# Optimization experiments

Measured on AMD Instinct MI355X. Metric: run time of the kernel, lower is better.

Reference implementation:

```python
import jax, jax.numpy as jnp
import numpy as np

FRAME_SIZE = 160

def _gru(x, h0, wih, whh, bih, bhh):
    # x: [B,T,D], h0: [B,U]; torch GRU gate order: r, z, n
    xp = jnp.einsum('btd,gd->btg', x, wih) + bih  # [B,T,3U]
    def step(h, xt):
        hp = h @ whh.T + bhh
        xr, xz, xn = jnp.split(xt, 3, axis=-1)
        hr, hz, hn = jnp.split(hp, 3, axis=-1)
        r = jax.nn.sigmoid(xr + hr)
        z = jax.nn.sigmoid(xz + hz)
        n = jnp.tanh(xn + r * hn)
        h_new = (1.0 - z) * n + z * h
        return h_new, h_new
    hT, ys = jax.lax.scan(step, h0, jnp.swapaxes(xp, 0, 1))
    return jnp.swapaxes(ys, 0, 1), hT

def _conv1d(x, w, b):
    # x: [B,C,T], w: [O,I,K], valid padding
    y = jax.lax.conv_general_dilated(x, w, (1,), 'VALID', dimension_numbers=('NCH', 'OIH', 'NCH'))
    return y + b[None, :, None]

def setup_inputs() -> dict:
    key = jax.random.key(0)
    ks = jax.random.split(key, 24)
    B, T, FD = 16, 36, 20
    PE, CD, K = 64, 128, 3
    SE, UA, UB, OUT = 128, 384, 64, 256
    NS = 3
    S = (T - 2 * (K - 1)) * FRAME_SIZE  # 32 * 160 = 5120
    s = 0.05
    inp = {
        'features': jax.random.normal(ks[0], (B, T, FD), jnp.float32),
        'periods': jax.random.randint(ks[1], (B, T, 1), 0, 256),
        'signals': jax.random.randint(ks[2], (B, S, NS), 0, 256),
        'gru_a_state': jnp.zeros((B, UA), jnp.float32),
        'gru_b_state': jnp.zeros((B, UB), jnp.float32),
        'period_emb': jax.random.normal(ks[3], (256, PE), jnp.float32) * s,
        'signal_emb': jax.random.normal(ks[4], (256, SE), jnp.float32) * s,
        'conv1_w': jax.random.normal(ks[5], (CD, FD + PE, K), jnp.float32) * s,
        'conv1_b': jnp.zeros((CD,), jnp.float32),
        'conv2_w': jax.random.normal(ks[6], (CD, CD, K), jnp.float32) * s,
        'conv2_b': jnp.zeros((CD,), jnp.float32),
        'fd1_w': jax.random.normal(ks[7], (CD, CD), jnp.float32) * s,
        'fd1_b': jnp.zeros((CD,), jnp.float32),
        'fd2_w': jax.random.normal(ks[8], (CD, CD), jnp.float32) * s,
        'fd2_b': jnp.zeros((CD,), jnp.float32),
        'grua_wih': jax.random.normal(ks[9], (3 * UA, NS * SE + CD), jnp.float32) * s,
        'grua_whh': jax.random.normal(ks[10], (3 * UA, UA), jnp.float32) * s,
        'grua_bih': jnp.zeros((3 * UA,), jnp.float32),
        'grua_bhh': jnp.zeros((3 * UA,), jnp.float32),
        'grub_wih': jax.random.normal(ks[11], (3 * UB, UA + CD), jnp.float32) * s,
        'grub_whh': jax.random.normal(ks[12], (3 * UB, UB), jnp.float32) * s,
        'grub_bih': jnp.zeros((3 * UB,), jnp.float32),
        'grub_bhh': jnp.zeros((3 * UB,), jnp.float32),
        'fc1_w': jax.random.normal(ks[13], (OUT, UB), jnp.float32) * s,
        'fc1_b': jnp.zeros((OUT,), jnp.float32),
        'fc2_w': jax.random.normal(ks[14], (OUT, UB), jnp.float32) * s,
        'fc2_b': jnp.zeros((OUT,), jnp.float32),
        'alpha': jnp.ones((OUT,), jnp.float32),
        'beta': jnp.ones((OUT,), jnp.float32),
    }
    return inp

def reference(features, periods, signals, gru_a_state, gru_b_state, period_emb,
              signal_emb, conv1_w, conv1_b, conv2_w, conv2_b, fd1_w, fd1_b,
              fd2_w, fd2_b, grua_wih, grua_whh, grua_bih, grua_bhh, grub_wih,
              grub_whh, grub_bih, grub_bhh, fc1_w, fc1_b, fc2_w, fc2_b, alpha, beta):
    B = features.shape[0]
    # ---- frame rate network ----
    ep = period_emb[periods].reshape(B, periods.shape[1], -1)  # [B,T,PE]
    f = jnp.concatenate([features, ep], axis=-1)               # [B,T,FD+PE]
    c = jnp.transpose(f, (0, 2, 1))                            # [B,C,T]
    c = jnp.tanh(_conv1d(c, conv1_w, conv1_b))
    c = jnp.tanh(_conv1d(c, conv2_w, conv2_b))
    c = jnp.transpose(c, (0, 2, 1))                            # [B,T-4,CD]
    c = jnp.tanh(c @ fd1_w.T + fd1_b)
    c = jnp.tanh(c @ fd2_w.T + fd2_b)
    # ---- sample rate network ----
    es = signal_emb[signals].reshape(B, signals.shape[1], -1)  # [B,S,NS*SE]
    c_up = jnp.repeat(c, FRAME_SIZE, axis=1)                   # [B,S,CD]
    y = jnp.concatenate([es, c_up], axis=-1)
    y, _ = _gru(y, gru_a_state, grua_wih, grua_whh, grua_bih, grua_bhh)
    y = jnp.concatenate([y, c_up], axis=-1)
    y, _ = _gru(y, gru_b_state, grub_wih, grub_whh, grub_bih, grub_bhh)
    # dual FC: alpha*tanh(W1 y + b1) + beta*tanh(W2 y + b2)
    y = alpha * jnp.tanh(y @ fc1_w.T + fc1_b) + beta * jnp.tanh(y @ fc2_w.T + fc2_b)
    return jax.nn.log_softmax(y, axis=-1)
```

## Files before the change

kernel.cpp:

```cpp
#include <hip/hip_runtime.h>

typedef unsigned short u16;
typedef unsigned int u32;
typedef unsigned long long u64;
typedef __attribute__((ext_vector_type(8))) short bf16x8;
typedef __attribute__((ext_vector_type(4))) float f32x4;

#define S_LEN 5120
#define UB 64
#define GA 1152
#define CAPP (1 << 16)
#define FASTCAP 3000
#define RING_WORDS (16 * 8 * 3 * 128)

__device__ __forceinline__ float bf2f(u16 u) { return __uint_as_float(((u32)u) << 16); }
__device__ __forceinline__ u16 f2bf(float f) {
    u32 x = __float_as_uint(f);
    return (u16)((x + 0x7fffu + ((x >> 16) & 1u)) >> 16);
}
__device__ __forceinline__ float blo(u32 w) { return __uint_as_float(w << 16); }
__device__ __forceinline__ float bhi(u32 w) { return __uint_as_float(w & 0xffff0000u); }
__device__ __forceinline__ float sigm(float x) { return 1.f / (1.f + __expf(-x)); }
__device__ __forceinline__ float tanh_(float x) { float e = __expf(2.f * x); return 1.f - 2.f / (e + 1.f); }

#if __has_builtin(__builtin_amdgcn_fdot2)
typedef _Float16 h2v __attribute__((ext_vector_type(2)));
__device__ __forceinline__ float dot2p(u32 w, u32 h, float acc) {
    return __builtin_amdgcn_fdot2(__builtin_bit_cast(h2v, w), __builtin_bit_cast(h2v, h), acc, false);
}
__device__ __forceinline__ u32 packpair(float a, float b) {
    u16 x = __builtin_bit_cast(u16, (_Float16)a);
    u16 y = __builtin_bit_cast(u16, (_Float16)b);
    return (u32)x | ((u32)y << 16);
}
__device__ __forceinline__ u16 pack1(float a) { return __builtin_bit_cast(u16, (_Float16)a); }
#else
__device__ __forceinline__ float dot2p(u32 w, u32 h, float acc) {
    acc = fmaf(blo(w), blo(h), acc);
    return fmaf(bhi(w), bhi(h), acc);
}
__device__ __forceinline__ u32 packpair(float a, float b) { return (u32)f2bf(a) | ((u32)f2bf(b) << 16); }
__device__ __forceinline__ u16 pack1(float a) { return f2bf(a); }
#endif

__device__ __forceinline__ u64 ald64(const u64* p) {
    return __hip_atomic_load(p, __ATOMIC_RELAXED, __HIP_MEMORY_SCOPE_AGENT);
}
__device__ __forceinline__ u32 ald32(const u32* p) {
    return __hip_atomic_load(p, __ATOMIC_RELAXED, __HIP_MEMORY_SCOPE_AGENT);
}
__device__ __forceinline__ void ast32(u32* p, u32 v) {
    __hip_atomic_store(p, v, __ATOMIC_RELAXED, __HIP_MEMORY_SCOPE_AGENT);
}
__device__ __forceinline__ u64 ld64_sc0(const u64* p) {
    u64 v;
    asm volatile("global_load_dwordx2 %0, %1, off sc0\n\ts_waitcnt vmcnt(0)"
                 : "=v"(v) : "v"(p) : "memory");
    return v;
}
__device__ __forceinline__ void st32_sc0(u32* p, u32 v) {
    asm volatile("global_store_dword %0, %1, off sc0" :: "v"(p), "v"(v) : "memory");
}
__device__ __forceinline__ void pub32(u32* fastp, u32* slowp, u32 v) {
    st32_sc0(fastp, v);
    ast32(slowp, v);
}
__device__ __forceinline__ u64 poll64(const u64* fastp, const u64* slowp, u32 tg,
                                      bool allowFast, int* fastEn, int* dead) {
    u64 v;
    if (allowFast && *fastEn) {
        for (int i = 0; i < FASTCAP; ++i) {
            v = ld64_sc0(fastp);
            if (((u32)v & 0xffffu) == tg && (((u32)(v >> 32)) & 0xffffu) == tg) return v;
        }
        *fastEn = 0;
    }
    int cnt = 0;
    for (;;) {
        v = ald64(slowp);
        if (((u32)v & 0xffffu) == tg && (((u32)(v >> 32)) & 0xffffu) == tg) return v;
        if (*dead || ++cnt > CAPP) { *dead = 1; return v; }
    }
}
__device__ __forceinline__ void wgbar() {
    __builtin_amdgcn_sched_barrier(0);
    asm volatile("s_waitcnt lgkmcnt(0)" ::: "memory");
    __builtin_amdgcn_s_barrier();
    __builtin_amdgcn_sched_barrier(0);
}

__global__ __launch_bounds__(256) void k_cvt(const float* __restrict__ src, u16* __restrict__ dst) {
    int i = blockIdx.x * 256 + threadIdx.x;
    dst[i] = f2bf(src[i]);
}

__global__ __launch_bounds__(128) void k_frame1(const float* __restrict__ features, const int* __restrict__ periods,
                                                const float* __restrict__ pemb, const float* __restrict__ w,
                                                const float* __restrict__ bias, float* __restrict__ c1) {
    __shared__ float fin[3][84];
    int t = blockIdx.x, b = blockIdx.y, o = threadIdx.x;
    for (int i = threadIdx.x; i < 252; i += 128) {
        int kk = i / 84, ci = i % 84, tt = t + kk;
        float v;
        if (ci < 20) v = features[(b * 36 + tt) * 20 + ci];
        else v = pemb[periods[b * 36 + tt] * 64 + (ci - 20)];
        fin[kk][ci] = v;
    }
    __syncthreads();
    float acc = bias[o];
    for (int kk = 0; kk < 3; kk++)
        for (int ci = 0; ci < 84; ci++)
            acc = fmaf(fin[kk][ci], w[o * 252 + ci * 3 + kk], acc);
    c1[(b * 34 + t) * 128 + o] = tanh_(acc);
}

__global__ __launch_bounds__(128) void k_frame2(const float* __restrict__ c1, const float* __restrict__ w,
                                                const float* __restrict__ bias, float* __restrict__ c2) {
    __shared__ float fin[3][128];
    int t = blockIdx.x, b = blockIdx.y, o = threadIdx.x;
    for (int i = threadIdx.x; i < 384; i += 128) {
        int kk = i >> 7, ci = i & 127;
        fin[kk][ci] = c1[(b * 34 + t + kk) * 128 + ci];
    }
    __syncthreads();
    float acc = bias[o];
    for (int kk = 0; kk < 3; kk++)
        for (int ci = 0; ci < 128; ci++)
            acc = fmaf(fin[kk][ci], w[o * 384 + ci * 3 + kk], acc);
    c2[(b * 32 + t) * 128 + o] = tanh_(acc);
}

__global__ __launch_bounds__(128) void k_fd(const float* __restrict__ c2, const float* __restrict__ w1,
                                            const float* __restrict__ b1, const float* __restrict__ w2,
                                            const float* __restrict__ b2, float* __restrict__ cc) {
    __shared__ float a0[128], a1s[128];
    int t = blockIdx.x, b = blockIdx.y, o = threadIdx.x;
    a0[o] = c2[(b * 32 + t) * 128 + o];
    __syncthreads();
    float acc = b1[o];
    for (int k = 0; k < 128; k++) acc = fmaf(a0[k], w1[o * 128 + k], acc);
    a1s[o] = tanh_(acc);
    __syncthreads();
    float acc2 = b2[o];
    for (int k = 0; k < 128; k++) acc2 = fmaf(a1s[k], w2[o * 128 + k], acc2);
    cc[(b * 32 + t) * 128 + o] = tanh_(acc2);
}

__global__ __launch_bounds__(192) void k_cpart(const float* __restrict__ cc, const float* __restrict__ wihB,
                                               const float* __restrict__ bihB, float* __restrict__ cpart) {
    __shared__ float cl[128];
    int fr = blockIdx.x, b = blockIdx.y, o = threadIdx.x;
    if (o < 128) cl[o] = cc[(b * 32 + fr) * 128 + o];
    __syncthreads();
    float acc = bihB[o];
    for (int k = 0; k < 128; k++) acc = fmaf(cl[k], wihB[o * 512 + 384 + k], acc);
    cpart[((size_t)b * 32 + fr) * 192 + o] = acc;
}

__global__ __launch_bounds__(256) void k_init(u32* base, int n) {
    int i = blockIdx.x * 256 + threadIdx.x;
    if (i < n) ast32(base + i, 0u);
}

__global__ __launch_bounds__(256) void k_gemm(const int* __restrict__ signals, const float* __restrict__ semb,
                                              const float* __restrict__ c, const u16* __restrict__ wih,
                                              const float* __restrict__ bih, u16* __restrict__ xp) {
    __shared__ u16 As[64][40];
    __shared__ u16 Bs[64][40];
    int m0 = blockIdx.x * 64, n0 = blockIdx.y * 64;
    int tid = threadIdx.x;
    int r = tid >> 2, kc = tid & 3;
    int lane = tid & 63, wv = tid >> 6;
    int wr = wv >> 1, wc = wv & 1;
    int mrow = m0 + r;
    int b = mrow / S_LEN, s = mrow % S_LEN;
    const int* sigrow = signals + mrow * 3;
    const float* crow = c + ((size_t)(b * 32) + s / 160) * 128;
    f32x4 acc[2][2];
#pragma unroll
    for (int i = 0; i < 2; i++)
#pragma unroll
        for (int j = 0; j < 2; j++) { acc[i][j][0] = 0.f; acc[i][j][1] = 0.f; acc[i][j][2] = 0.f; acc[i][j][3] = 0.f; }
    for (int k0 = 0; k0 < 512; k0 += 32) {
        int k = k0 + kc * 8;
        float v[8];
        if (k < 384) {
            int idx = sigrow[k >> 7];
            const float* src = semb + idx * 128 + (k & 127);
#pragma unroll
            for (int j = 0; j < 8; j++) v[j] = src[j];
        } else {
            const float* src = crow + (k - 384);
#pragma unroll
            for (int j = 0; j < 8; j++) v[j] = src[j];
        }
        u32 pk[4];
#pragma unroll
        for (int j = 0; j < 4; j++) pk[j] = (u32)f2bf(v[2 * j]) | ((u32)f2bf(v[2 * j + 1]) << 16);
        *(uint4*)&As[r][kc * 8] = *(uint4*)pk;
        *(uint4*)&Bs[r][kc * 8] = *(const uint4*)&wih[(size_t)(n0 + r) * 512 + k];
        __syncthreads();
        bf16x8 af[2], bfr[2];
#pragma unroll
        for (int mi = 0; mi < 2; mi++) af[mi] = *(const bf16x8*)&As[wr * 32 + mi * 16 + (lane & 15)][(lane >> 4) * 8];
#pragma unroll
        for (int ni = 0; ni < 2; ni++) bfr[ni] = *(const bf16x8*)&Bs[wc * 32 + ni * 16 + (lane & 15)][(lane >> 4) * 8];
#pragma unroll
        for (int mi = 0; mi < 2; mi++)
#pragma unroll
            for (int ni = 0; ni < 2; ni++)
                acc[mi][ni] = __builtin_amdgcn_mfma_f32_16x16x32_bf16(af[mi], bfr[ni], acc[mi][ni], 0, 0, 0);
        __syncthreads();
    }
#pragma unroll
    for (int mi = 0; mi < 2; mi++)
#pragma unroll
        for (int ni = 0; ni < 2; ni++) {
            int row = m0 + wr * 32 + mi * 16 + (lane >> 4) * 4;
            int col = n0 + wc * 32 + ni * 16 + (lane & 15);
            float bias = bih[col];
#pragma unroll
            for (int i = 0; i < 4; i++)
                xp[(size_t)(row + i) * GA + col] = f2bf(acc[mi][ni][i] + bias);
        }
}

__global__ __launch_bounds__(512) void k_serial(
        const float* __restrict__ whhA, const float* __restrict__ bhhA,
        const float* __restrict__ wihB, const float* __restrict__ whhB,
        const float* __restrict__ bhhB, const u16* __restrict__ xp,
        const float* __restrict__ cpart, const float* __restrict__ h0a,
        const float* __restrict__ h0b, u32* hExF, u32* hExS, u32* bprog,
        float* __restrict__ yB) {
    const int blk = blockIdx.x, tid = threadIdx.x;
    const int b = (blk & 7) | ((blk >> 5) << 3);
    const int role = (blk >> 3) & 3;

    if (role < 3) {
        __shared__ __align__(16) u32 hbuf[2][192];
        __shared__ float red[384][5];
        __shared__ u16 xpb[2][384];
        __shared__ int lbB, deadf, fastEn;
        const int s = role;
        const int u = tid & 127, kc = tid >> 7;
        u32 w[3][64];
        if (tid < 384) {
#pragma unroll
            for (int g = 0; g < 3; g++) {
                const float* wr = whhA + ((size_t)(g * 384 + s * 128 + u)) * 384 + kc * 128;
#pragma unroll
                for (int c = 0; c < 16; c++)
#pragma unroll
                    for (int j = 0; j < 4; j++)
                        w[g][c * 4 + j] = packpair(wr[c * 8 + 2 * j], wr[c * 8 + 2 * j + 1]);
            }
        }
        if (tid < 192) hbuf[0][tid] = packpair(h0a[b * 384 + 2 * tid], h0a[b * 384 + 2 * tid + 1]);
        const int j1 = tid - 128;
        const int xcol1 = (tid >= 128 && tid < 512) ? ((j1 >> 7) * 384 + s * 128 + (j1 & 127)) : 0;
        const int j2 = tid + 128;
        const int xcol2 = (tid >= 128 && tid < 256) ? ((j2 >> 7) * 384 + s * 128 + (j2 & 127)) : 0;
        float hprA = 0, bh0 = 0, bh1 = 0, bh2 = 0;
        if (tid < 128) {
            hprA = h0a[b * 384 + s * 128 + tid];
            bh0 = bhhA[s * 128 + tid];
            bh1 = bhhA[384 + s * 128 + tid];
            bh2 = bhhA[768 + s * 128 + tid];
        }
        if (tid >= 128 && tid < 384) xpb[0][j1] = xp[((size_t)b * S_LEN) * GA + xcol1];
        if (tid >= 128 && tid < 256) xpb[0][j2] = xp[((size_t)b * S_LEN) * GA + xcol2];
        if (tid == 0) { lbB = 0; deadf = 0; fastEn = 1; }
        __syncthreads();

        for (int t = 0; t < S_LEN; ++t) {
            const int p = t & 1, p2 = p ^ 1;
            const bool hasx = (t + 1 < S_LEN);
            u16 xq1 = 0, xq2 = 0;
            int lbn = -1;
            if (tid >= 384) {
                if (t > 0) {
                    const int i = tid - 384, pi = i >> 6, idx = i & 63;
                    const int ps = pi + (pi >= s ? 1 : 0);
                    const size_t woff = (((size_t)b * 8 + ((t - 1) & 7)) * 3 + ps) * 64 + idx;
                    u64 v = poll64((const u64*)hExF + woff, (const u64*)hExS + woff,
                                   (u32)t & 0xffffu, t >= 2, &fastEn, &deadf);
                    hbuf[p][ps * 64 + idx] = (((u32)v) >> 16) | (((u32)(v >> 32)) & 0xffff0000u);
                }
            } else if (tid >= 128) {
                if (hasx) {
                    xq1 = xp[((size_t)b * S_LEN + t + 1) * GA + xcol1];
                    if (tid < 256) xq2 = xp[((size_t)b * S_LEN + t + 1) * GA + xcol2];
                }
                if (tid == 383 && (t & 3) == 0) lbn = (int)ald32(bprog + b);
            }
            wgbar();
            if (tid < 384) {
                const uint4* hb4 = (const uint4*)&hbuf[p][0] + kc * 16;
                float a00 = 0, a01 = 0, a10 = 0, a11 = 0, a20 = 0, a21 = 0;
#pragma unroll
                for (int c = 0; c < 16; c++) {
                    uint4 hc = hb4[c];
                    a00 = dot2p(w[0][4 * c + 0], hc.x, a00); a01 = dot2p(w[0][4 * c + 1], hc.y, a01);
                    a00 = dot2p(w[0][4 * c + 2], hc.z, a00); a01 = dot2p(w[0][4 * c + 3], hc.w, a01);
                    a10 = dot2p(w[1][4 * c + 0], hc.x, a10); a11 = dot2p(w[1][4 * c + 1], hc.y, a11);
                    a10 = dot2p(w[1][4 * c + 2], hc.z, a10); a11 = dot2p(w[1][4 * c + 3], hc.w, a11);
                    a20 = dot2p(w[2][4 * c + 0], hc.x, a20); a21 = dot2p(w[2][4 * c + 1], hc.y, a21);
                    a20 = dot2p(w[2][4 * c + 2], hc.z, a20); a21 = dot2p(w[2][4 * c + 3], hc.w, a21);
                }
                red[u][kc] = a00 + a01;
                red[128 + u][kc] = a10 + a11;
                red[256 + u][kc] = a20 + a21;
            }
            if (hasx && tid >= 128 && tid < 384) {
                xpb[p2][j1] = xq1;
                if (tid < 256) xpb[p2][j2] = xq2;
            }
            if (tid == 383 && lbn >= 0) lbB = lbn;
            wgbar();
            if (tid < 128) {
                float pr = red[tid][0] + red[tid][1] + red[tid][2] + bh0;
                float pz = red[128 + tid][0] + red[128 + tid][1] + red[128 + tid][2] + bh1;
                float pn = red[256 + tid][0] + red[256 + tid][1] + red[256 + tid][2] + bh2;
                float rg = sigm(bf2f(xpb[p][tid]) + pr);
                float zg = sigm(bf2f(xpb[p][128 + tid]) + pz);
                float ng = tanh_(bf2f(xpb[p][256 + tid]) + rg * pn);
                float hnew = (1.f - zg) * ng + zg * hprA;
                hprA = hnew;
                u16 hb16 = pack1(hnew);
                ((u16*)&hbuf[p2][0])[s * 128 + tid] = hb16;
                if (t - 7 > lbB && !deadf) {
                    int cnt = 0;
                    while ((int)ald32(bprog + b) < t - 7) {
                        if (++cnt > CAPP) { deadf = 1; break; }
                    }
                }
                const size_t poff = (((size_t)b * 8 + (t & 7)) * 3 + s) * 128 + tid;
                pub32(hExF + poff, hExS + poff, ((u32)hb16 << 16) | (u32)(t + 1));
            }
        }
    } else {
        __shared__ __align__(16) u32 hbufA[192];
        __shared__ __align__(16) u16 hbB[2][64];
        __shared__ float redy[192][3];
        __shared__ float redh[192];
        __shared__ float cpl[32][192];
        __shared__ int deadB, fastEnB;
        const int r = (tid < 192) ? tid : tid - 192;
        const int kh = (tid < 192) ? 0 : 1;
        u32 wy[96];
        if (tid < 384) {
            const float* wr = wihB + (size_t)r * 512 + kh * 192;
#pragma unroll
            for (int i = 0; i < 96; i++) wy[i] = packpair(wr[2 * i], wr[2 * i + 1]);
        }
        u32 wb0[32], wb1[32];
        if (tid >= 384 && tid < 480) {
            const int rb = (tid - 384) * 2;
            const float* w0p = whhB + (size_t)rb * 64;
            const float* w1p = whhB + (size_t)(rb + 1) * 64;
#pragma unroll
            for (int i = 0; i < 32; i++) {
                wb0[i] = packpair(w0p[2 * i], w0p[2 * i + 1]);
                wb1[i] = packpair(w1p[2 * i], w1p[2 * i + 1]);
            }
        }
        for (int i = tid; i < 32 * 192; i += 512)
            cpl[i / 192][i % 192] = cpart[((size_t)b * 32) * 192 + i];
        float bB0 = 0, bB1 = 0, bB2 = 0, hprB = 0;
        if (tid < 64) {
            bB0 = bhhB[tid]; bB1 = bhhB[64 + tid]; bB2 = bhhB[128 + tid];
            hprB = h0b[b * 64 + tid];
            hbB[0][tid] = pack1(hprB);
        }
        if (tid == 0) { deadB = 0; fastEnB = 1; }
        __syncthreads();

        for (int tb = 0; tb < S_LEN; ++tb) {
            const int p = tb & 1, p2 = p ^ 1;
            if (tid >= 192 && tid < 384) {
                const int i = tid - 192, ps = i >> 6, idx = i & 63;
                const size_t woff = (((size_t)b * 8 + (tb & 7)) * 3 + ps) * 64 + idx;
                u64 v = poll64((const u64*)hExF + woff, (const u64*)hExS + woff,
                               (u32)(tb + 1) & 0xffffu, tb >= 1, &fastEnB, &deadB);
                hbufA[ps * 64 + idx] = (((u32)v) >> 16) | (((u32)(v >> 32)) & 0xffff0000u);
            }
            wgbar();
            if (tid < 384) {
                const uint4* hb4 = (const uint4*)&hbufA[0] + kh * 24;
                float a0 = 0, a1 = 0;
#pragma unroll
                for (int c = 0; c < 24; c++) {
                    uint4 hc = hb4[c];
                    a0 = dot2p(wy[4 * c + 0], hc.x, a0); a1 = dot2p(wy[4 * c + 1], hc.y, a1);
                    a0 = dot2p(wy[4 * c + 2], hc.z, a0); a1 = dot2p(wy[4 * c + 3], hc.w, a1);
                }
                redy[r][kh] = a0 + a1;
            } else if (tid < 480) {
                const uint4* hb4 = (const uint4*)&hbB[p][0];
                float a0 = 0, b0 = 0;
#pragma unroll
                for (int q = 0; q < 8; q++) {
                    uint4 hc = hb4[q];
                    a0 = dot2p(wb0[4 * q + 0], hc.x, a0); a0 = dot2p(wb0[4 * q + 1], hc.y, a0);
                    a0 = dot2p(wb0[4 * q + 2], hc.z, a0); a0 = dot2p(wb0[4 * q + 3], hc.w, a0);
                    b0 = dot2p(wb1[4 * q + 0], hc.x, b0); b0 = dot2p(wb1[4 * q + 1], hc.y, b0);
                    b0 = dot2p(wb1[4 * q + 2], hc.z, b0); b0 = dot2p(wb1[4 * q + 3], hc.w, b0);
                }
                const int rb = (tid - 384) * 2;
                redh[rb] = a0;
                redh[rb + 1] = b0;
            }
            wgbar();
            if (tid < 64) {
                const int fr = tb / 160;
                float xr = redy[tid][0] + redy[tid][1] + cpl[fr][tid];
                float xz = redy[64 + tid][0] + redy[64 + tid][1] + cpl[fr][64 + tid];
                float xn = redy[128 + tid][0] + redy[128 + tid][1] + cpl[fr][128 + tid];
                float hr = redh[tid] + bB0;
                float hz = redh[64 + tid] + bB1;
                float hn = redh[128 + tid] + bB2;
                float rg = sigm(xr + hr);
                float zg = sigm(xz + hz);
                float ng = tanh_(xn + rg * hn);
                float hnew = (1.f - zg) * ng + zg * hprB;
                hprB = hnew;
                hbB[p2][tid] = pack1(hnew);
                yB[((size_t)b * S_LEN + tb) * UB + tid] = hnew;
                if (tid == 0) ast32(bprog + b, (u32)(tb + 1));
            }
        }
    }
}

__global__ __launch_bounds__(256) void k_fc(const float* __restrict__ yB, const float* __restrict__ w1,
                                            const float* __restrict__ b1, const float* __restrict__ w2,
                                            const float* __restrict__ b2, const float* __restrict__ alpha,
                                            const float* __restrict__ beta, float* __restrict__ out) {
    __shared__ float yb[4][64];
    __shared__ float vb[4][256];
    int tid = threadIdx.x;
    size_t r0 = (size_t)blockIdx.x * 4;
    { int r = tid >> 6, k = tid & 63; yb[r][k] = yB[(r0 + r) * 64 + k]; }
    __syncthreads();
    int o = tid;
    float a1[4] = {0, 0, 0, 0}, a2[4] = {0, 0, 0, 0};
    for (int k = 0; k < 64; k += 4) {
        float4 u = *(const float4*)(w1 + o * 64 + k);
        float4 v = *(const float4*)(w2 + o * 64 + k);
#pragma unroll
        for (int r = 0; r < 4; r++) {
            float y0 = yb[r][k], y1 = yb[r][k + 1], y2 = yb[r][k + 2], y3 = yb[r][k + 3];
            a1[r] = fmaf(u.x, y0, fmaf(u.y, y1, fmaf(u.z, y2, fmaf(u.w, y3, a1[r]))));
            a2[r] = fmaf(v.x, y0, fmaf(v.y, y1, fmaf(v.z, y2, fmaf(v.w, y3, a2[r]))));
        }
    }
    float al = alpha[o], be = beta[o], c1 = b1[o], c2 = b2[o];
#pragma unroll
    for (int r = 0; r < 4; r++)
        vb[r][o] = al * tanh_(a1[r] + c1) + be * tanh_(a2[r] + c2);
    __syncthreads();
    int wv = tid >> 6, l = tid & 63;
    float x0 = vb[wv][l], x1 = vb[wv][64 + l], x2 = vb[wv][128 + l], x3 = vb[wv][192 + l];
    float m = fmaxf(fmaxf(x0, x1), fmaxf(x2, x3));
#pragma unroll
    for (int off = 1; off < 64; off <<= 1) m = fmaxf(m, __shfl_xor(m, off));
    float sum = __expf(x0 - m) + __expf(x1 - m) + __expf(x2 - m) + __expf(x3 - m);
#pragma unroll
    for (int off = 1; off < 64; off <<= 1) sum += __shfl_xor(sum, off);
    float lse = m + __logf(sum);
    float* po = out + (r0 + wv) * 256;
    po[l] = x0 - lse;
    po[64 + l] = x1 - lse;
    po[128 + l] = x2 - lse;
    po[192 + l] = x3 - lse;
}

extern "C" void kernel_launch(void* const* d_in, const int* in_sizes, int n_in,
                              void* d_out, int out_size, void* d_ws, size_t ws_size,
                              hipStream_t stream) {
    const float* features = (const float*)d_in[0];
    const int* periods = (const int*)d_in[1];
    const int* signals = (const int*)d_in[2];
    const float* gruA0 = (const float*)d_in[3];
    const float* gruB0 = (const float*)d_in[4];
    const float* period_emb = (const float*)d_in[5];
    const float* signal_emb = (const float*)d_in[6];
    const float* conv1_w = (const float*)d_in[7];
    const float* conv1_b = (const float*)d_in[8];
    const float* conv2_w = (const float*)d_in[9];
    const float* conv2_b = (const float*)d_in[10];
    const float* fd1_w = (const float*)d_in[11];
    const float* fd1_b = (const float*)d_in[12];
    const float* fd2_w = (const float*)d_in[13];
    const float* fd2_b = (const float*)d_in[14];
    const float* grua_wih = (const float*)d_in[15];
    const float* grua_whh = (const float*)d_in[16];
    const float* grua_bih = (const float*)d_in[17];
    const float* grua_bhh = (const float*)d_in[18];
    const float* grub_wih = (const float*)d_in[19];
    const float* grub_whh = (const float*)d_in[20];
    const float* grub_bih = (const float*)d_in[21];
    const float* grub_bhh = (const float*)d_in[22];
    const float* fc1_w = (const float*)d_in[23];
    const float* fc1_b = (const float*)d_in[24];
    const float* fc2_w = (const float*)d_in[25];
    const float* fc2_b = (const float*)d_in[26];
    const float* alpha = (const float*)d_in[27];
    const float* beta = (const float*)d_in[28];
    float* out = (float*)d_out;

    char* ws = (char*)d_ws;
    size_t off = 0;
    auto alloc = [&](size_t bytes) { void* p = ws + off; off += (bytes + 255) & ~(size_t)255; return p; };
    u16* xp = (u16*)alloc((size_t)16 * 5120 * 1152 * 2);
    u16* wihA = (u16*)alloc((size_t)1152 * 512 * 2);
    float* c1 = (float*)alloc((size_t)16 * 34 * 128 * 4);
    float* c2 = (float*)alloc((size_t)16 * 32 * 128 * 4);
    float* cc = (float*)alloc((size_t)16 * 32 * 128 * 4);
    float* cpart = (float*)alloc((size_t)16 * 32 * 192 * 4);
    float* yB = (float*)alloc((size_t)16 * 5120 * 64 * 4);
    u32* hExF = (u32*)alloc((size_t)RING_WORDS * 4);
    u32* hExS = (u32*)alloc((size_t)(RING_WORDS + 256) * 4);
    u32* bprog = hExS + RING_WORDS;
    const int initN = 2 * RING_WORDS + 256;

    k_cvt<<<dim3(2304), dim3(256), 0, stream>>>(grua_wih, wihA);
    k_frame1<<<dim3(34, 16), dim3(128), 0, stream>>>(features, periods, period_emb, conv1_w, conv1_b, c1);
    k_frame2<<<dim3(32, 16), dim3(128), 0, stream>>>(c1, conv2_w, conv2_b, c2);
    k_fd<<<dim3(32, 16), dim3(128), 0, stream>>>(c2, fd1_w, fd1_b, fd2_w, fd2_b, cc);
    k_cpart<<<dim3(32, 16), dim3(192), 0, stream>>>(cc, grub_wih, grub_bih, cpart);
    k_init<<<dim3((initN + 255) / 256), dim3(256), 0, stream>>>(hExF, initN);
    k_gemm<<<dim3(1280, 18), dim3(256), 0, stream>>>(signals, signal_emb, cc, wihA, grua_bih, xp);
    k_serial<<<dim3(64), dim3(512), 0, stream>>>(grua_whh, grua_bhh, grub_wih, grub_whh, grub_bhh,
                                                 xp, cpart, gruA0, gruB0, hExF, hExS, bprog, yB);
    k_fc<<<dim3(20480), dim3(256), 0, stream>>>(yB, fc1_w, fc1_b, fc2_w, fc2_b, alpha, beta, out);
}
```

Before: 10.20 ms.

## Split GRU-A recurrence across six workgroups per batch instead of three

The persistent serial kernel now splits GRU-A's hidden state into six 64-unit slices per batch element instead of three 128-unit slices. The grid grows from 64 to 112 workgroups, and the exchange ring layout changes to 6x64. Each workgroup holds 96 packed weight registers instead of 192, and the per-step dot product splits into two K-chunks of 192. This is meant to shorten each step's critical-path compute and ease register pressure, at the cost of more cross-workgroup h exchange and polling (five peers instead of two) every timestep.

```diff
diff --git a/kernel.cpp b/kernel.cpp
--- a/kernel.cpp
+++ b/kernel.cpp
@@ -11,7 +11,7 @@
 #define GA 1152
 #define CAPP (1 << 16)
 #define FASTCAP 3000
-#define RING_WORDS (16 * 8 * 3 * 128)
+#define RING_WORDS (16 * 8 * 6 * 64)
 
 __device__ __forceinline__ float bf2f(u16 u) { return __uint_as_float(((u32)u) << 16); }
 __device__ __forceinline__ u16 f2bf(float f) {
@@ -233,108 +233,90 @@
         const float* __restrict__ h0b, u32* hExF, u32* hExS, u32* bprog,
         float* __restrict__ yB) {
     const int blk = blockIdx.x, tid = threadIdx.x;
-    const int b = (blk & 7) | ((blk >> 5) << 3);
-    const int role = (blk >> 3) & 3;
-
-    if (role < 3) {
+    const int q = blk >> 3;
+    const int role = q % 7;
+    const int b = (blk & 7) | ((q / 7) << 3);
+
+    if (role < 6) {
         __shared__ __align__(16) u32 hbuf[2][192];
-        __shared__ float red[384][5];
-        __shared__ u16 xpb[2][384];
+        __shared__ float red[192][5];
+        __shared__ u16 xpb[2][192];
         __shared__ int lbB, deadf, fastEn;
         const int s = role;
-        const int u = tid & 127, kc = tid >> 7;
-        u32 w[3][64];
+        const int rr = tid % 192, kc = tid / 192;
+        u32 w[96];
         if (tid < 384) {
-#pragma unroll
-            for (int g = 0; g < 3; g++) {
-                const float* wr = whhA + ((size_t)(g * 384 + s * 128 + u)) * 384 + kc * 128;
-#pragma unroll
-                for (int c = 0; c < 16; c++)
-#pragma unroll
-                    for (int j = 0; j < 4; j++)
-                        w[g][c * 4 + j] = packpair(wr[c * 8 + 2 * j], wr[c * 8 + 2 * j + 1]);
-            }
+            const int G = (rr >> 6) * 384 + s * 64 + (rr & 63);
+            const float* wr = whhA + (size_t)G * 384 + kc * 192;
+#pragma unroll
+            for (int i = 0; i < 96; i++) w[i] = packpair(wr[2 * i], wr[2 * i + 1]);
         }
         if (tid < 192) hbuf[0][tid] = packpair(h0a[b * 384 + 2 * tid], h0a[b * 384 + 2 * tid + 1]);
-        const int j1 = tid - 128;
-        const int xcol1 = (tid >= 128 && tid < 512) ? ((j1 >> 7) * 384 + s * 128 + (j1 & 127)) : 0;
-        const int j2 = tid + 128;
-        const int xcol2 = (tid >= 128 && tid < 256) ? ((j2 >> 7) * 384 + s * 128 + (j2 & 127)) : 0;
+        const int j = tid - 128;
+        const int xcol = (tid >= 128 && tid < 320) ? ((j >> 6) * 384 + s * 64 + (j & 63)) : 0;
         float hprA = 0, bh0 = 0, bh1 = 0, bh2 = 0;
-        if (tid < 128) {
-            hprA = h0a[b * 384 + s * 128 + tid];
-            bh0 = bhhA[s * 128 + tid];
-            bh1 = bhhA[384 + s * 128 + tid];
-            bh2 = bhhA[768 + s * 128 + tid];
-        }
-        if (tid >= 128 && tid < 384) xpb[0][j1] = xp[((size_t)b * S_LEN) * GA + xcol1];
-        if (tid >= 128 && tid < 256) xpb[0][j2] = xp[((size_t)b * S_LEN) * GA + xcol2];
+        if (tid < 64) {
+            hprA = h0a[b * 384 + s * 64 + tid];
+            bh0 = bhhA[s * 64 + tid];
+            bh1 = bhhA[384 + s * 64 + tid];
+            bh2 = bhhA[768 + s * 64 + tid];
+        }
+        if (tid >= 128 && tid < 320) xpb[0][j] = xp[((size_t)b * S_LEN) * GA + xcol];
         if (tid == 0) { lbB = 0; deadf = 0; fastEn = 1; }
         __syncthreads();
 
         for (int t = 0; t < S_LEN; ++t) {
             const int p = t & 1, p2 = p ^ 1;
             const bool hasx = (t + 1 < S_LEN);
-            u16 xq1 = 0, xq2 = 0;
+            u16 xq = 0;
             int lbn = -1;
-            if (tid >= 384) {
+            if (tid >= 352) {
                 if (t > 0) {
-                    const int i = tid - 384, pi = i >> 6, idx = i & 63;
+                    const int i = tid - 352, pi = i >> 5, k = i & 31;
                     const int ps = pi + (pi >= s ? 1 : 0);
-                    const size_t woff = (((size_t)b * 8 + ((t - 1) & 7)) * 3 + ps) * 64 + idx;
+                    const size_t woff = (((size_t)b * 8 + ((t - 1) & 7)) * 6 + ps) * 32 + k;
                     u64 v = poll64((const u64*)hExF + woff, (const u64*)hExS + woff,
                                    (u32)t & 0xffffu, t >= 2, &fastEn, &deadf);
-                    hbuf[p][ps * 64 + idx] = (((u32)v) >> 16) | (((u32)(v >> 32)) & 0xffff0000u);
+                    hbuf[p][ps * 32 + k] = (((u32)v) >> 16) | (((u32)(v >> 32)) & 0xffff0000u);
                 }
-            } else if (tid >= 128) {
-                if (hasx) {
-                    xq1 = xp[((size_t)b * S_LEN + t + 1) * GA + xcol1];
-                    if (tid < 256) xq2 = xp[((size_t)b * S_LEN + t + 1) * GA + xcol2];
-                }
-                if (tid == 383 && (t & 3) == 0) lbn = (int)ald32(bprog + b);
+            } else if (tid >= 128 && tid < 320) {
+                if (hasx) xq = xp[((size_t)b * S_LEN + t + 1) * GA + xcol];
+            } else if (tid == 320) {
+                if ((t & 3) == 0) lbn = (int)ald32(bprog + b);
             }
             wgbar();
             if (tid < 384) {
-                const uint4* hb4 = (const uint4*)&hbuf[p][0] + kc * 16;
-                float a00 = 0, a01 = 0, a10 = 0, a11 = 0, a20 = 0, a21 = 0;
-#pragma unroll
-                for (int c = 0; c < 16; c++) {
+                const uint4* hb4 = (const uint4*)&hbuf[p][0] + kc * 24;
+                float a0 = 0, a1 = 0;
+#pragma unroll
+                for (int c = 0; c < 24; c++) {
                     uint4 hc = hb4[c];
-                    a00 = dot2p(w[0][4 * c + 0], hc.x, a00); a01 = dot2p(w[0][4 * c + 1], hc.y, a01);
-                    a00 = dot2p(w[0][4 * c + 2], hc.z, a00); a01 = dot2p(w[0][4 * c + 3], hc.w, a01);
-                    a10 = dot2p(w[1][4 * c + 0], hc.x, a10); a11 = dot2p(w[1][4 * c + 1], hc.y, a11);
-                    a10 = dot2p(w[1][4 * c + 2], hc.z, a10); a11 = dot2p(w[1][4 * c + 3], hc.w, a11);
-                    a20 = dot2p(w[2][4 * c + 0], hc.x, a20); a21 = dot2p(w[2][4 * c + 1], hc.y, a21);
-                    a20 = dot2p(w[2][4 * c + 2], hc.z, a20); a21 = dot2p(w[2][4 * c + 3], hc.w, a21);
+                    a0 = dot2p(w[4 * c + 0], hc.x, a0); a1 = dot2p(w[4 * c + 1], hc.y, a1);
+                    a0 = dot2p(w[4 * c + 2], hc.z, a0); a1 = dot2p(w[4 * c + 3], hc.w, a1);
                 }
-                red[u][kc] = a00 + a01;
-                red[128 + u][kc] = a10 + a11;
-                red[256 + u][kc] = a20 + a21;
-            }
-            if (hasx && tid >= 128 && tid < 384) {
-                xpb[p2][j1] = xq1;
-                if (tid < 256) xpb[p2][j2] = xq2;
-            }
-            if (tid == 383 && lbn >= 0) lbB = lbn;
+                red[rr][kc] = a0 + a1;
+            }
+            if (hasx && tid >= 128 && tid < 320) xpb[p2][j] = xq;
+            if (tid == 320 && lbn >= 0) lbB = lbn;
             wgbar();
-            if (tid < 128) {
-                float pr = red[tid][0] + red[tid][1] + red[tid][2] + bh0;
-                float pz = red[128 + tid][0] + red[128 + tid][1] + red[128 + tid][2] + bh1;
-                float pn = red[256 + tid][0] + red[256 + tid][1] + red[256 + tid][2] + bh2;
+            if (tid < 64) {
+                float pr = red[tid][0] + red[tid][1] + bh0;
+                float pz = red[64 + tid][0] + red[64 + tid][1] + bh1;
+                float pn = red[128 + tid][0] + red[128 + tid][1] + bh2;
                 float rg = sigm(bf2f(xpb[p][tid]) + pr);
-                float zg = sigm(bf2f(xpb[p][128 + tid]) + pz);
-                float ng = tanh_(bf2f(xpb[p][256 + tid]) + rg * pn);
+                float zg = sigm(bf2f(xpb[p][64 + tid]) + pz);
+                float ng = tanh_(bf2f(xpb[p][128 + tid]) + rg * pn);
                 float hnew = (1.f - zg) * ng + zg * hprA;
                 hprA = hnew;
                 u16 hb16 = pack1(hnew);
-                ((u16*)&hbuf[p2][0])[s * 128 + tid] = hb16;
+                ((u16*)&hbuf[p2][0])[s * 64 + tid] = hb16;
                 if (t - 7 > lbB && !deadf) {
                     int cnt = 0;
                     while ((int)ald32(bprog + b) < t - 7) {
                         if (++cnt > CAPP) { deadf = 1; break; }
                     }
                 }
-                const size_t poff = (((size_t)b * 8 + (t & 7)) * 3 + s) * 128 + tid;
+                const size_t poff = (((size_t)b * 8 + (t & 7)) * 6 + s) * 64 + tid;
                 pub32(hExF + poff, hExS + poff, ((u32)hb16 << 16) | (u32)(t + 1));
             }
         }
@@ -378,11 +360,11 @@
         for (int tb = 0; tb < S_LEN; ++tb) {
             const int p = tb & 1, p2 = p ^ 1;
             if (tid >= 192 && tid < 384) {
-                const int i = tid - 192, ps = i >> 6, idx = i & 63;
-                const size_t woff = (((size_t)b * 8 + (tb & 7)) * 3 + ps) * 64 + idx;
+                const int i = tid - 192, ps = i >> 5, k = i & 31;
+                const size_t woff = (((size_t)b * 8 + (tb & 7)) * 6 + ps) * 32 + k;
                 u64 v = poll64((const u64*)hExF + woff, (const u64*)hExS + woff,
                                (u32)(tb + 1) & 0xffffu, tb >= 1, &fastEnB, &deadB);
-                hbufA[ps * 64 + idx] = (((u32)v) >> 16) | (((u32)(v >> 32)) & 0xffff0000u);
+                hbufA[ps * 32 + k] = (((u32)v) >> 16) | (((u32)(v >> 32)) & 0xffff0000u);
             }
             wgbar();
             if (tid < 384) {
@@ -399,12 +381,12 @@
                 const uint4* hb4 = (const uint4*)&hbB[p][0];
                 float a0 = 0, b0 = 0;
 #pragma unroll
-                for (int q = 0; q < 8; q++) {
-                    uint4 hc = hb4[q];
-                    a0 = dot2p(wb0[4 * q + 0], hc.x, a0); a0 = dot2p(wb0[4 * q + 1], hc.y, a0);
-                    a0 = dot2p(wb0[4 * q + 2], hc.z, a0); a0 = dot2p(wb0[4 * q + 3], hc.w, a0);
-                    b0 = dot2p(wb1[4 * q + 0], hc.x, b0); b0 = dot2p(wb1[4 * q + 1], hc.y, b0);
-                    b0 = dot2p(wb1[4 * q + 2], hc.z, b0); b0 = dot2p(wb1[4 * q + 3], hc.w, b0);
+                for (int qq = 0; qq < 8; qq++) {
+                    uint4 hc = hb4[qq];
+                    a0 = dot2p(wb0[4 * qq + 0], hc.x, a0); a0 = dot2p(wb0[4 * qq + 1], hc.y, a0);
+                    a0 = dot2p(wb0[4 * qq + 2], hc.z, a0); a0 = dot2p(wb0[4 * qq + 3], hc.w, a0);
+                    b0 = dot2p(wb1[4 * qq + 0], hc.x, b0); b0 = dot2p(wb1[4 * qq + 1], hc.y, b0);
+                    b0 = dot2p(wb1[4 * qq + 2], hc.z, b0); b0 = dot2p(wb1[4 * qq + 3], hc.w, b0);
                 }
                 const int rb = (tid - 384) * 2;
                 redh[rb] = a0;
@@ -531,7 +513,7 @@
     k_cpart<<<dim3(32, 16), dim3(192), 0, stream>>>(cc, grub_wih, grub_bih, cpart);
     k_init<<<dim3((initN + 255) / 256), dim3(256), 0, stream>>>(hExF, initN);
     k_gemm<<<dim3(1280, 18), dim3(256), 0, stream>>>(signals, signal_emb, cc, wihA, grua_bih, xp);
-    k_serial<<<dim3(64), dim3(512), 0, stream>>>(grua_whh, grua_bhh, grub_wih, grub_whh, grub_bhh,
-                                                 xp, cpart, gruA0, gruB0, hExF, hExS, bprog, yB);
+    k_serial<<<dim3(112), dim3(512), 0, stream>>>(grua_whh, grua_bhh, grub_wih, grub_whh, grub_bhh,
+                                                  xp, cpart, gruA0, gruB0, hExF, hExS, bprog, yB);
     k_fc<<<dim3(20480), dim3(256), 0, stream>>>(yB, fc1_w, fc1_b, fc2_w, fc2_b, alpha, beta, out);
 }
```

Measured after the change: 8.762 ms. 14.1% less time.
